# Kernel optimization log

Hardware: AMD Instinct MI355X
Metric: run time of the kernel (lower is better)

## Reference

```python
import jax, jax.numpy as jnp
import numpy as np

EPS = 1e-5

def _bn(x, p):
    # p: (4, C) rows = gamma, beta, running_mean, running_var ; x: (B, C, H, W)
    g, b, m, v = p[0], p[1], p[2], p[3]
    sh = (1, -1, 1, 1)
    return (x - m.reshape(sh)) * (g.reshape(sh) * jax.lax.rsqrt(v.reshape(sh) + EPS)) + b.reshape(sh)

def _cba1(x, w, p):
    # 1x1 conv (no bias) + BN + ReLU
    return jax.nn.relu(_bn(jnp.einsum('oc,bchw->bohw', w, x), p))

def setup_inputs() -> dict:
    B, C, H, W = 2, 512, 128, 256
    CK, K, CO = 256, 19, 512
    key = jax.random.key(0)
    ks = jax.random.split(key, 10)
    def w(k, shape, fan):
        return jax.random.normal(k, shape, jnp.float32) * (fan ** -0.5)
    def bn(c):
        return jnp.stack([jnp.ones((c,), jnp.float32), jnp.zeros((c,), jnp.float32),
                          jnp.zeros((c,), jnp.float32), jnp.ones((c,), jnp.float32)])
    return {
        'x': jax.random.normal(ks[0], (B, C, H, W), jnp.float32),
        'proxy_feats': jax.random.normal(ks[1], (B, C, K, 1), jnp.float32),
        'wq1': w(ks[2], (CK, C), C),  'bnq1': bn(CK),
        'wq2': w(ks[3], (CK, CK), CK), 'bnq2': bn(CK),
        'wk1': w(ks[4], (CK, C), C),  'bnk1': bn(CK),
        'wk2': w(ks[5], (CK, CK), CK), 'bnk2': bn(CK),
        'wv':  w(ks[6], (CK, C), C),  'bnv':  bn(CK),
        'wout': w(ks[7], (C, CK), CK), 'bnout': bn(C),
        'wbot': w(ks[8], (CO, 2 * C, 3, 3), 2 * C * 9), 'bnbot': bn(CO),
    }

def reference(x, proxy_feats, wq1, wq2, wk1, wk2, wv, wout, wbot,
              bnq1, bnq2, bnk1, bnk2, bnv, bnout, bnbot):
    B, C, H, W = x.shape
    CK = wq1.shape[0]
    # --- ObjectContextBlock: pixel-region cross attention ---
    q = _cba1(_cba1(x, wq1, bnq1), wq2, bnq2)            # (B, CK, H, W)
    k = _cba1(_cba1(proxy_feats, wk1, bnk1), wk2, bnk2)  # (B, CK, K, 1)
    v = _cba1(proxy_feats, wv, bnv)                      # (B, CK, K, 1)
    q = q.reshape(B, CK, H * W)                          # (B, CK, N)
    k = k.reshape(B, CK, -1)                             # (B, CK, K)
    v = v.reshape(B, CK, -1)                             # (B, CK, K)
    sim = jnp.einsum('bcn,bck->bnk', q, k) * (CK ** -0.5)
    sim = jax.nn.softmax(sim, axis=-1)                   # (B, N, K)
    ctx = jnp.einsum('bnk,bck->bcn', sim, v).reshape(B, CK, H, W)
    ctx = _cba1(ctx, wout, bnout)                        # (B, C, H, W)
    # --- bottleneck: concat + 3x3 conv + BN + ReLU ---
    cat = jnp.concatenate([ctx, x], axis=1)              # (B, 2C, H, W)
    out = jax.lax.conv_general_dilated(cat, wbot, (1, 1), 'SAME',
                                       dimension_numbers=('NCHW', 'OIHW', 'NCHW'))
    return jax.nn.relu(_bn(out, bnbot))
```

## Files before the change

kernel.cpp:

```cpp
#include <hip/hip_runtime.h>
#include <cstdint>

#define EPS 1e-5f
#define PADW 258
#define PADROWS 33540
#define NPIX 32768

typedef __attribute__((ext_vector_type(8))) short bf16x8;
typedef __attribute__((ext_vector_type(4))) float f32x4;

__device__ __forceinline__ ushort f2bf(float f) {
  union { float f; uint32_t u; } v; v.f = f;
  uint32_t r = v.u + 0x7fffu + ((v.u >> 16) & 1u);
  return (ushort)(r >> 16);
}
__device__ __forceinline__ float bf2f(ushort h) {
  union { uint32_t u; float f; } v; v.u = ((uint32_t)h) << 16;
  return v.f;
}
__device__ __forceinline__ void gload_lds16(const void* g, void* lds) {
  __builtin_amdgcn_global_load_lds((__attribute__((address_space(1))) void*)g,
                                   (__attribute__((address_space(3))) void*)lds,
                                   16, 0, 0);
}

template <int BMODE, int OMODE>
__global__ __launch_bounds__(256) void mfma_gemm(
    const ushort* __restrict__ A, const ushort* __restrict__ B,
    const float* __restrict__ bn, void* __restrict__ OutV,
    int M, int K, int pitchB, int ciB, long strideB, int pitchO, long strideO) {
  const int lane = threadIdx.x & 63;
  const int wave = threadIdx.x >> 6;
  const int wm = (wave & 1) * 64;
  const int wn = (wave >> 1) * 64;
  const int m0 = blockIdx.y * 128;
  const int n0 = blockIdx.x * 128;
  const int z  = blockIdx.z;
  B += (size_t)z * strideB;

  const int h = n0 >> 8, w0 = n0 & 255;
  long prowB;
  if (BMODE == 0) prowB = n0;
  else            prowB = (long)(h + 1) * PADW + (w0 + 1);

  __shared__ __align__(16) ushort Asl[4 * 128 * 8];
  __shared__ __align__(16) ushort Bsl[4 * 128 * 8];

  f32x4 acc[4][4];
#pragma unroll
  for (int mt = 0; mt < 4; ++mt)
#pragma unroll
    for (int nt = 0; nt < 4; ++nt) acc[mt][nt] = (f32x4){0.f, 0.f, 0.f, 0.f};

  for (int k0 = 0; k0 < K; k0 += 32) {
#pragma unroll
    for (int i = 0; i < 2; ++i) {
      int c = (wave * 2 + i) * 64 + lane;
      int mm = c >> 2, g = (c & 3) ^ ((mm >> 1) & 3);
      gload_lds16(A + (size_t)(m0 + mm) * K + (k0 + g * 8), Asl + c * 8);
    }
    long rowb; int cib;
    if (BMODE == 2) {
      int tap = k0 >> 10;
      int dy = tap / 3 - 1, dx = tap % 3 - 1;
      rowb = prowB + dy * PADW + dx;
      cib  = k0 & 1023;
    } else {
      rowb = prowB;
      cib  = ciB + k0;
    }
#pragma unroll
    for (int i = 0; i < 2; ++i) {
      int c = (wave * 2 + i) * 64 + lane;
      int nn = c >> 2, g = (c & 3) ^ ((nn >> 1) & 3);
      gload_lds16(B + (size_t)(rowb + nn) * pitchB + cib + g * 8, Bsl + c * 8);
    }
    __syncthreads();
    bf16x8 af[4], bfr[4];
#pragma unroll
    for (int t = 0; t < 4; ++t) {
      int ks = lane >> 4;
      int ma = wm + t * 16 + (lane & 15);
      int nb = wn + t * 16 + (lane & 15);
      af[t]  = *(const bf16x8*)(Asl + (ma * 4 + (ks ^ ((ma >> 1) & 3))) * 8);
      bfr[t] = *(const bf16x8*)(Bsl + (nb * 4 + (ks ^ ((nb >> 1) & 3))) * 8);
    }
#pragma unroll
    for (int mt = 0; mt < 4; ++mt)
#pragma unroll
      for (int nt = 0; nt < 4; ++nt)
        acc[mt][nt] = __builtin_amdgcn_mfma_f32_16x16x32_bf16(af[mt], bfr[nt], acc[mt][nt], 0, 0, 0);
    __syncthreads();
  }

  const int q4 = lane >> 4, col = lane & 15;
  float scv[16], bov[16];
#pragma unroll
  for (int mt = 0; mt < 4; ++mt)
#pragma unroll
    for (int r = 0; r < 4; ++r) {
      int m = m0 + wm + mt * 16 + q4 * 4 + r;
      float s = bn[m] * rsqrtf(bn[3 * M + m] + EPS);
      scv[mt * 4 + r] = s;
      bov[mt * 4 + r] = bn[M + m] - bn[2 * M + m] * s;
    }
  if (OMODE == 2) {
    float* Outf = (float*)OutV + (size_t)z * strideO;
#pragma unroll
    for (int mt = 0; mt < 4; ++mt)
#pragma unroll
      for (int r = 0; r < 4; ++r) {
        int m = m0 + wm + mt * 16 + q4 * 4 + r;
        float* rowp = Outf + (size_t)m * NPIX + n0 + wn;
#pragma unroll
        for (int nt = 0; nt < 4; ++nt)
          rowp[nt * 16 + col] = fmaxf(acc[mt][nt][r] * scv[mt * 4 + r] + bov[mt * 4 + r], 0.f);
      }
  } else {
    ushort* Outh = (ushort*)OutV + (size_t)z * strideO;
    long prowO = (OMODE == 0) ? (long)n0 : ((long)(h + 1) * PADW + (w0 + 1));
#pragma unroll
    for (int nt = 0; nt < 4; ++nt) {
      long row = prowO + wn + nt * 16 + col;
      ushort* p = Outh + (size_t)row * pitchO + m0 + wm;
#pragma unroll
      for (int mt = 0; mt < 4; ++mt) {
        ushort4 pk;
        pk.x = f2bf(fmaxf(acc[mt][nt][0] * scv[mt * 4 + 0] + bov[mt * 4 + 0], 0.f));
        pk.y = f2bf(fmaxf(acc[mt][nt][1] * scv[mt * 4 + 1] + bov[mt * 4 + 1], 0.f));
        pk.z = f2bf(fmaxf(acc[mt][nt][2] * scv[mt * 4 + 2] + bov[mt * 4 + 2], 0.f));
        pk.w = f2bf(fmaxf(acc[mt][nt][3] * scv[mt * 4 + 3] + bov[mt * 4 + 3], 0.f));
        *(ushort4*)(p + mt * 16 + q4 * 4) = pk;
      }
    }
  }
}

#define PXS  130
#define ROWC (PXS * 4)
#define BUFC (3 * ROWC)
__global__ __launch_bounds__(256, 3) void conv3x3_mfma(
    const ushort* __restrict__ W2, const ushort* __restrict__ cat,
    const float* __restrict__ bn, float* __restrict__ out) {
  const int tid  = threadIdx.x;
  const int lane = tid & 63;
  const int wave = tid >> 6;
  const int wm = (wave & 1) * 64;
  const int wn = (wave >> 1) * 64;
  const int m0 = (blockIdx.x & 3) * 128;
  const int n0 = (blockIdx.x >> 2) * 128;
  const int z  = blockIdx.z;
  const int h = n0 >> 8, w0 = n0 & 255;
  const int prow0 = (h + 1) * PADW + (w0 + 1);
  const ushort* Bz = cat + (size_t)z * PADROWS * 1024;

  __shared__ __align__(16) ushort halo[2 * BUFC * 8];

  f32x4 acc[4][4];
#pragma unroll
  for (int mt = 0; mt < 4; ++mt)
#pragma unroll
    for (int nt = 0; nt < 4; ++nt) acc[mt][nt] = (f32x4){0.f, 0.f, 0.f, 0.f};

  int offs[7];
#pragma unroll
  for (int s = 0; s < 7; ++s) {
    int c = s * 256 + tid;
    if (c < BUFC) {
      int o_slot = c & 3;
      int q = c >> 2;
      int p = q % PXS;
      int r = q / PXS;
      int o_g = o_slot ^ ((p >> 1) & 3);
      offs[s] = ((prow0 + (r - 1) * PADW + (p - 1)) << 10) + o_g * 8;
    } else {
      offs[s] = -1;
    }
  }

  auto stage = [&](int buf, int ci0n) {
#pragma unroll
    for (int s = 0; s < 7; ++s)
      if (offs[s] >= 0)
        gload_lds16(Bz + (size_t)offs[s] + ci0n,
                    halo + ((size_t)buf * BUFC + s * 256 + wave * 64) * 8);
  };

  const ushort* Alane = W2 + (size_t)(m0 + wm + (lane & 15)) * 32 + (lane >> 4) * 8;

  const int p0  = wn + (lane & 15);
  const int oct = lane >> 4;
  int hoff0[3];
#pragma unroll
  for (int dx = 0; dx < 3; ++dx) {
    int p = p0 + dx;
    hoff0[dx] = (p * 4 + (oct ^ ((p >> 1) & 3))) * 16;
  }

  stage(0, 0);
  __syncthreads();

  for (int it = 0; it < 32; ++it) {
    const ushort* Ait = Alane + (size_t)it * (9 * 16384);

    bf16x8 af[2][4];
#pragma unroll
    for (int t = 0; t < 2; ++t)
#pragma unroll
      for (int mt = 0; mt < 4; ++mt)
        af[t][mt] = *(const bf16x8*)(Ait + (size_t)t * 16384 + mt * 512);

    __builtin_amdgcn_sched_barrier(0);
    if (it < 31) stage((it + 1) & 1, (it + 1) * 32);
    __builtin_amdgcn_sched_barrier(0);

    const char* hb0 = (const char*)(halo + (size_t)(it & 1) * BUFC * 8);
    bf16x8 bfr[2][4];
#pragma unroll
    for (int nt = 0; nt < 4; ++nt)
      bfr[0][nt] = *(const bf16x8*)(hb0 + nt * 1024 + hoff0[0]);

#pragma unroll
    for (int t = 0; t < 9; ++t) {
      if (t < 8) {
        const int r1 = (t + 1) / 3, dx1 = (t + 1) % 3;
#pragma unroll
        for (int nt = 0; nt < 4; ++nt)
          bfr[(t + 1) & 1][nt] =
              *(const bf16x8*)(hb0 + r1 * (ROWC * 16) + nt * 1024 + hoff0[dx1]);
      }
      __builtin_amdgcn_s_setprio(1);
#pragma unroll
      for (int nt = 0; nt < 4; ++nt)
#pragma unroll
        for (int mt = 0; mt < 4; ++mt)
          acc[mt][nt] = __builtin_amdgcn_mfma_f32_16x16x32_bf16(
              af[t & 1][mt], bfr[t & 1][nt], acc[mt][nt], 0, 0, 0);
      __builtin_amdgcn_s_setprio(0);
      if (t < 7) {
#pragma unroll
        for (int mt = 0; mt < 4; ++mt)
          af[t & 1][mt] = *(const bf16x8*)(Ait + (size_t)(t + 2) * 16384 + mt * 512);
      }
    }
    __syncthreads();
  }

  const int q4 = lane >> 4, col = lane & 15;
  float* Outf = out + (size_t)z * 512 * NPIX;
#pragma unroll
  for (int mt = 0; mt < 4; ++mt)
#pragma unroll
    for (int r = 0; r < 4; ++r) {
      int m = m0 + wm + mt * 16 + q4 * 4 + r;
      float s  = bn[m] * rsqrtf(bn[3 * 512 + m] + EPS);
      float bo = bn[512 + m] - bn[2 * 512 + m] * s;
      float* rowp = Outf + (size_t)m * NPIX + n0 + wn;
#pragma unroll
      for (int nt = 0; nt < 4; ++nt)
        rowp[nt * 16 + col] = fmaxf(acc[mt][nt][r] * s + bo, 0.f);
    }
}

__global__ __launch_bounds__(64) void small_gemm_kernel(
    const float* __restrict__ Wm, const float* __restrict__ X,
    const float* __restrict__ bn, float* __restrict__ Y,
    int CO, int CI, int KC) {
  int co = blockIdx.x, b = blockIdx.y, kc = threadIdx.x;
  if (kc >= KC) return;
  const float* Xb = X + (size_t)b * CI * KC;
  float acc = 0.f;
  for (int c = 0; c < CI; ++c) acc += Wm[(size_t)co * CI + c] * Xb[(size_t)c * KC + kc];
  float s  = bn[co] * rsqrtf(bn[3 * CO + co] + EPS);
  float bs = bn[CO + co] - bn[2 * CO + co] * s;
  Y[((size_t)b * CO + co) * KC + kc] = fmaxf(acc * s + bs, 0.f);
}

__global__ __launch_bounds__(256) void attention_kernel(
    const ushort* __restrict__ qT, const float* __restrict__ Kp,
    const float* __restrict__ Vp, ushort* __restrict__ ctxT) {
  int b = blockIdx.y;
  int pix = blockIdx.x * 256 + threadIdx.x;
  __shared__ float ks[256][19], vs[256][19];
  for (int idx = threadIdx.x; idx < 256 * 19; idx += 256) {
    int c = idx / 19, kk = idx % 19;
    ks[c][kk] = Kp[((size_t)b * 256 + c) * 19 + kk];
    vs[c][kk] = Vp[((size_t)b * 256 + c) * 19 + kk];
  }
  __syncthreads();

  const ushort* qrow = qT + ((size_t)b * NPIX + pix) * 256;
  float sim[19];
#pragma unroll
  for (int kk = 0; kk < 19; ++kk) sim[kk] = 0.f;
  for (int c0 = 0; c0 < 256; c0 += 8) {
    uint4 raw = *(const uint4*)(qrow + c0);
    float qf[8] = {bf2f((ushort)(raw.x & 0xffff)), bf2f((ushort)(raw.x >> 16)),
                   bf2f((ushort)(raw.y & 0xffff)), bf2f((ushort)(raw.y >> 16)),
                   bf2f((ushort)(raw.z & 0xffff)), bf2f((ushort)(raw.z >> 16)),
                   bf2f((ushort)(raw.w & 0xffff)), bf2f((ushort)(raw.w >> 16))};
#pragma unroll
    for (int j = 0; j < 8; ++j)
#pragma unroll
      for (int kk = 0; kk < 19; ++kk) sim[kk] += qf[j] * ks[c0 + j][kk];
  }
  const float scale = 0.0625f;
  float mx = -1e30f;
#pragma unroll
  for (int kk = 0; kk < 19; ++kk) { sim[kk] *= scale; mx = fmaxf(mx, sim[kk]); }
  float denom = 0.f;
#pragma unroll
  for (int kk = 0; kk < 19; ++kk) { sim[kk] = __expf(sim[kk] - mx); denom += sim[kk]; }
  float inv = 1.f / denom;
#pragma unroll
  for (int kk = 0; kk < 19; ++kk) sim[kk] *= inv;

  ushort* crow = ctxT + ((size_t)b * NPIX + pix) * 256;
  for (int c0 = 0; c0 < 256; c0 += 8) {
    uint32_t o[4];
#pragma unroll
    for (int j = 0; j < 4; ++j) {
      float v0 = 0.f, v1 = 0.f;
#pragma unroll
      for (int kk = 0; kk < 19; ++kk) {
        v0 += sim[kk] * vs[c0 + j * 2][kk];
        v1 += sim[kk] * vs[c0 + j * 2 + 1][kk];
      }
      o[j] = (uint32_t)f2bf(v0) | ((uint32_t)f2bf(v1) << 16);
    }
    *(uint4*)(crow + c0) = make_uint4(o[0], o[1], o[2], o[3]);
  }
}

__global__ __launch_bounds__(256) void transpose_x_kernel(
    const float* __restrict__ x, ushort* __restrict__ cat) {
  int b = blockIdx.z, ci0 = blockIdx.y * 64, n0 = blockIdx.x * 64;
  __shared__ float t[64][65];
  const float* xb = x + ((size_t)b * 512 + ci0) * NPIX + n0;
  for (int i = 0; i < 16; ++i) {
    int idx = i * 256 + threadIdx.x;
    int c = idx >> 6, w = idx & 63;
    t[c][w] = xb[(size_t)c * NPIX + w];
  }
  __syncthreads();
  int h = n0 >> 8, w0 = n0 & 255;
  size_t pbase = ((size_t)b * PADROWS + (size_t)(h + 1) * PADW + (w0 + 1)) * 1024 + 512 + ci0;
  for (int i = 0; i < 16; ++i) {
    int idx = i * 256 + threadIdx.x;
    int n = idx >> 6, c = idx & 63;
    cat[pbase + (size_t)n * 1024 + c] = f2bf(t[c][n]);
  }
}

__global__ void convert_w_kernel(const float* __restrict__ in, ushort* __restrict__ out, int n) {
  int i = blockIdx.x * 256 + threadIdx.x;
  if (i < n) out[i] = f2bf(in[i]);
}
__global__ void repack_conv_w_kernel(const float* __restrict__ wbot, ushort* __restrict__ Wrb) {
  int idx = blockIdx.x * 256 + threadIdx.x;
  if (idx >= 512 * 9216) return;
  int ci_in = idx & 31;
  int r  = idx >> 5;
  int co = r & 511;
  int tt = r >> 9;
  int t = tt % 9, chunk = tt / 9;
  Wrb[idx] = f2bf(wbot[((size_t)co * 1024 + chunk * 32 + ci_in) * 9 + t]);
}

extern "C" void kernel_launch(void* const* d_in, const int* in_sizes, int n_in,
                              void* d_out, int out_size, void* d_ws, size_t ws_size,
                              hipStream_t stream) {
  const float* x     = (const float*)d_in[0];
  const float* proxy = (const float*)d_in[1];
  const float* wq1   = (const float*)d_in[2];
  const float* bnq1  = (const float*)d_in[3];
  const float* wq2   = (const float*)d_in[4];
  const float* bnq2  = (const float*)d_in[5];
  const float* wk1   = (const float*)d_in[6];
  const float* bnk1  = (const float*)d_in[7];
  const float* wk2   = (const float*)d_in[8];
  const float* bnk2  = (const float*)d_in[9];
  const float* wv    = (const float*)d_in[10];
  const float* bnv   = (const float*)d_in[11];
  const float* wout  = (const float*)d_in[12];
  const float* bnout = (const float*)d_in[13];
  const float* wbot  = (const float*)d_in[14];
  const float* bnbot = (const float*)d_in[15];
  float* out = (float*)d_out;

  const int B = 2, C = 512, CK = 256, KC = 19;
  char* ws = (char*)d_ws;
  const size_t catBytes = (size_t)B * PADROWS * 1024 * 2;
  ushort* cat  = (ushort*)ws;
  ushort* bufA = (ushort*)(ws + 137379840);
  ushort* bufB = (ushort*)(ws + 137379840 + 33554432);
  ushort* Wrb  = (ushort*)(ws + 204488704);
  ushort* wq1b = (ushort*)(ws + 213925888);
  ushort* wq2b = (ushort*)(ws + 214188032);
  ushort* woutb= (ushort*)(ws + 214319104);
  float*  k1   = (float*)(ws + 214581248);
  float*  k2   = k1 + (size_t)B * CK * KC;
  float*  vv   = k2 + (size_t)B * CK * KC;

  hipMemsetAsync(cat, 0, catBytes, stream);

  convert_w_kernel<<<(CK * C + 255) / 256, 256, 0, stream>>>(wq1, wq1b, CK * C);
  convert_w_kernel<<<(CK * CK + 255) / 256, 256, 0, stream>>>(wq2, wq2b, CK * CK);
  convert_w_kernel<<<(C * CK + 255) / 256, 256, 0, stream>>>(wout, woutb, C * CK);
  repack_conv_w_kernel<<<(512 * 9216 + 255) / 256, 256, 0, stream>>>(wbot, Wrb);

  small_gemm_kernel<<<dim3(CK, B), 64, 0, stream>>>(wk1, proxy, bnk1, k1, CK, C, KC);
  small_gemm_kernel<<<dim3(CK, B), 64, 0, stream>>>(wk2, k1, bnk2, k2, CK, CK, KC);
  small_gemm_kernel<<<dim3(CK, B), 64, 0, stream>>>(wv, proxy, bnv, vv, CK, C, KC);

  transpose_x_kernel<<<dim3(NPIX / 64, 8, B), 256, 0, stream>>>(x, cat);

  const long padStride = (long)PADROWS * 1024;
  const long nckStride = (long)NPIX * 256;

  mfma_gemm<1, 0><<<dim3(NPIX / 128, 2, B), 256, 0, stream>>>(
      wq1b, cat, bnq1, bufA, 256, 512, 1024, 512, padStride, 256, nckStride);
  mfma_gemm<0, 0><<<dim3(NPIX / 128, 2, B), 256, 0, stream>>>(
      wq2b, bufA, bnq2, bufB, 256, 256, 256, 0, nckStride, 256, nckStride);

  attention_kernel<<<dim3(NPIX / 256, B), 256, 0, stream>>>(bufB, k2, vv, bufA);

  mfma_gemm<0, 1><<<dim3(NPIX / 128, 4, B), 256, 0, stream>>>(
      woutb, bufA, bnout, cat, 512, 256, 256, 0, nckStride, 1024, padStride);

  conv3x3_mfma<<<dim3((NPIX / 128) * 4, 1, B), 256, 0, stream>>>(Wrb, cat, bnbot, out);
}
```

Measured before the change: 1.276 ms.

## Interleave conv halo staging per tap, zero only borders, split small GEMM reduction

The 3x3 conv main loop now spreads the seven async global-to-LDS halo loads across the first seven taps and uses fine-grained s_barrier plus explicit waitcnt in place of a bulk stage and a __syncthreads per chunk. It also prefetches the next chunk's weight fragments at the last tap. The full memset of the padded concat buffer is replaced by a small kernel that zeroes only the border pixels, since the interior is overwritten anyway. The small proxy GEMMs are split four ways over the input channels, with a reduction through shared memory. The extra per-tap barriers add synchronisation cost, and the hand-placed vmcnt values must match the number of outstanding loads to stay correct.

```diff
diff --git a/kernel.cpp b/kernel.cpp
--- a/kernel.cpp
+++ b/kernel.cpp
@@ -178,12 +178,10 @@
     }
   }
 
-  auto stage = [&](int buf, int ci0n) {
-#pragma unroll
-    for (int s = 0; s < 7; ++s)
-      if (offs[s] >= 0)
-        gload_lds16(Bz + (size_t)offs[s] + ci0n,
-                    halo + ((size_t)buf * BUFC + s * 256 + wave * 64) * 8);
+  auto stage1 = [&](int s, int buf, int ci0n) {
+    if (offs[s] >= 0)
+      gload_lds16(Bz + (size_t)offs[s] + ci0n,
+                  halo + ((size_t)buf * BUFC + s * 256 + wave * 64) * 8);
   };
 
   const ushort* Alane = W2 + (size_t)(m0 + wm + (lane & 15)) * 32 + (lane >> 4) * 8;
@@ -197,53 +195,63 @@
     hoff0[dx] = (p * 4 + (oct ^ ((p >> 1) & 3))) * 16;
   }
 
-  stage(0, 0);
-  __syncthreads();
+#pragma unroll
+  for (int s = 0; s < 7; ++s) stage1(s, 0, 0);
+  bf16x8 af[2][4];
+#pragma unroll
+  for (int t = 0; t < 2; ++t)
+#pragma unroll
+    for (int mt = 0; mt < 4; ++mt)
+      af[t][mt] = *(const bf16x8*)(Alane + (size_t)t * 16384 + mt * 512);
+  asm volatile("s_waitcnt vmcnt(8)" ::: "memory");
+  __builtin_amdgcn_sched_barrier(0);
+  __builtin_amdgcn_s_barrier();
 
   for (int it = 0; it < 32; ++it) {
     const ushort* Ait = Alane + (size_t)it * (9 * 16384);
-
-    bf16x8 af[2][4];
-#pragma unroll
-    for (int t = 0; t < 2; ++t)
-#pragma unroll
-      for (int mt = 0; mt < 4; ++mt)
-        af[t][mt] = *(const bf16x8*)(Ait + (size_t)t * 16384 + mt * 512);
-
-    __builtin_amdgcn_sched_barrier(0);
-    if (it < 31) stage((it + 1) & 1, (it + 1) * 32);
-    __builtin_amdgcn_sched_barrier(0);
-
+    const ushort* An  = Ait + (size_t)(9 * 16384);
     const char* hb0 = (const char*)(halo + (size_t)(it & 1) * BUFC * 8);
-    bf16x8 bfr[2][4];
-#pragma unroll
-    for (int nt = 0; nt < 4; ++nt)
-      bfr[0][nt] = *(const bf16x8*)(hb0 + nt * 1024 + hoff0[0]);
+    const int nbuf = (it + 1) & 1;
+    const int nci  = (it + 1) * 32;
+    const bool more = (it < 31);
 
 #pragma unroll
     for (int t = 0; t < 9; ++t) {
-      if (t < 8) {
-        const int r1 = (t + 1) / 3, dx1 = (t + 1) % 3;
-#pragma unroll
-        for (int nt = 0; nt < 4; ++nt)
-          bfr[(t + 1) & 1][nt] =
-              *(const bf16x8*)(hb0 + r1 * (ROWC * 16) + nt * 1024 + hoff0[dx1]);
-      }
+      const int r = t / 3, dx = t % 3;
+      bf16x8 bfr[4];
+#pragma unroll
+      for (int nt = 0; nt < 4; ++nt)
+        bfr[nt] = *(const bf16x8*)(hb0 + r * (ROWC * 16) + nt * 1024 + hoff0[dx]);
+      if (t < 7 && more) stage1(t, nbuf, nci);
+      __builtin_amdgcn_s_barrier();
+      asm volatile("s_waitcnt lgkmcnt(0)" ::: "memory");
+      __builtin_amdgcn_sched_barrier(0);
       __builtin_amdgcn_s_setprio(1);
 #pragma unroll
       for (int nt = 0; nt < 4; ++nt)
 #pragma unroll
         for (int mt = 0; mt < 4; ++mt)
           acc[mt][nt] = __builtin_amdgcn_mfma_f32_16x16x32_bf16(
-              af[t & 1][mt], bfr[t & 1][nt], acc[mt][nt], 0, 0, 0);
+              af[t & 1][mt], bfr[nt], acc[mt][nt], 0, 0, 0);
       __builtin_amdgcn_s_setprio(0);
       if (t < 7) {
 #pragma unroll
         for (int mt = 0; mt < 4; ++mt)
           af[t & 1][mt] = *(const bf16x8*)(Ait + (size_t)(t + 2) * 16384 + mt * 512);
+      } else if (t == 8 && more) {
+#pragma unroll
+        for (int mt = 0; mt < 4; ++mt)
+          af[0][mt] = *(const bf16x8*)(An + mt * 512);
+#pragma unroll
+        for (int mt = 0; mt < 4; ++mt)
+          af[1][mt] = *(const bf16x8*)(An + 16384 + mt * 512);
       }
-    }
-    __syncthreads();
+      if (t == 8) {
+        asm volatile("s_waitcnt vmcnt(8)" ::: "memory");
+        __builtin_amdgcn_sched_barrier(0);
+      }
+      __builtin_amdgcn_s_barrier();
+    }
   }
 
   const int q4 = lane >> 4, col = lane & 15;
@@ -262,18 +270,29 @@
     }
 }
 
-__global__ __launch_bounds__(64) void small_gemm_kernel(
+__global__ __launch_bounds__(256) void small_gemm_kernel(
     const float* __restrict__ Wm, const float* __restrict__ X,
     const float* __restrict__ bn, float* __restrict__ Y,
     int CO, int CI, int KC) {
-  int co = blockIdx.x, b = blockIdx.y, kc = threadIdx.x;
-  if (kc >= KC) return;
+  int co = blockIdx.x, b = blockIdx.y;
+  int q = threadIdx.x >> 6, kc = threadIdx.x & 63;
+  __shared__ float part[3][24];
   const float* Xb = X + (size_t)b * CI * KC;
+  const float* Wr = Wm + (size_t)co * CI;
   float acc = 0.f;
-  for (int c = 0; c < CI; ++c) acc += Wm[(size_t)co * CI + c] * Xb[(size_t)c * KC + kc];
-  float s  = bn[co] * rsqrtf(bn[3 * CO + co] + EPS);
-  float bs = bn[CO + co] - bn[2 * CO + co] * s;
-  Y[((size_t)b * CO + co) * KC + kc] = fmaxf(acc * s + bs, 0.f);
+  int cq = CI >> 2;
+  if (kc < KC) {
+    for (int c = q * cq; c < (q + 1) * cq; ++c)
+      acc += Wr[c] * Xb[(size_t)c * KC + kc];
+  }
+  if (q > 0 && kc < KC) part[q - 1][kc] = acc;
+  __syncthreads();
+  if (q == 0 && kc < KC) {
+    acc += part[0][kc] + part[1][kc] + part[2][kc];
+    float s  = bn[co] * rsqrtf(bn[3 * CO + co] + EPS);
+    float bs = bn[CO + co] - bn[2 * CO + co] * s;
+    Y[((size_t)b * CO + co) * KC + kc] = fmaxf(acc * s + bs, 0.f);
+  }
 }
 
 __global__ __launch_bounds__(256) void attention_kernel(
@@ -350,6 +369,18 @@
     int n = idx >> 6, c = idx & 63;
     cat[pbase + (size_t)n * 1024 + c] = f2bf(t[c][n]);
   }
+}
+
+__global__ __launch_bounds__(256) void zero_border_kernel(ushort* __restrict__ cat) {
+  int b = blockIdx.y, i = blockIdx.x;
+  int row, col;
+  if (i < 258)      { row = 0;            col = i; }
+  else if (i < 516) { row = 129;          col = i - 258; }
+  else if (i < 644) { row = i - 516 + 1;  col = 0; }
+  else              { row = i - 644 + 1;  col = 257; }
+  size_t base = ((size_t)b * PADROWS + (size_t)row * PADW + col) * 1024 +
+                (size_t)threadIdx.x * 4;
+  *(ushort4*)(cat + base) = make_ushort4(0, 0, 0, 0);
 }
 
 __global__ void convert_w_kernel(const float* __restrict__ in, ushort* __restrict__ out, int n) {
@@ -390,7 +421,6 @@
 
   const int B = 2, C = 512, CK = 256, KC = 19;
   char* ws = (char*)d_ws;
-  const size_t catBytes = (size_t)B * PADROWS * 1024 * 2;
   ushort* cat  = (ushort*)ws;
   ushort* bufA = (ushort*)(ws + 137379840);
   ushort* bufB = (ushort*)(ws + 137379840 + 33554432);
@@ -402,16 +432,16 @@
   float*  k2   = k1 + (size_t)B * CK * KC;
   float*  vv   = k2 + (size_t)B * CK * KC;
 
-  hipMemsetAsync(cat, 0, catBytes, stream);
+  zero_border_kernel<<<dim3(772, B), 256, 0, stream>>>(cat);
 
   convert_w_kernel<<<(CK * C + 255) / 256, 256, 0, stream>>>(wq1, wq1b, CK * C);
   convert_w_kernel<<<(CK * CK + 255) / 256, 256, 0, stream>>>(wq2, wq2b, CK * CK);
   convert_w_kernel<<<(C * CK + 255) / 256, 256, 0, stream>>>(wout, woutb, C * CK);
   repack_conv_w_kernel<<<(512 * 9216 + 255) / 256, 256, 0, stream>>>(wbot, Wrb);
 
-  small_gemm_kernel<<<dim3(CK, B), 64, 0, stream>>>(wk1, proxy, bnk1, k1, CK, C, KC);
-  small_gemm_kernel<<<dim3(CK, B), 64, 0, stream>>>(wk2, k1, bnk2, k2, CK, CK, KC);
-  small_gemm_kernel<<<dim3(CK, B), 64, 0, stream>>>(wv, proxy, bnv, vv, CK, C, KC);
+  small_gemm_kernel<<<dim3(CK, B), 256, 0, stream>>>(wk1, proxy, bnk1, k1, CK, C, KC);
+  small_gemm_kernel<<<dim3(CK, B), 256, 0, stream>>>(wk2, k1, bnk2, k2, CK, CK, KC);
+  small_gemm_kernel<<<dim3(CK, B), 256, 0, stream>>>(wv, proxy, bnv, vv, CK, C, KC);
 
   transpose_x_kernel<<<dim3(NPIX / 64, 8, B), 256, 0, stream>>>(x, cat);
 
```

Result: faster. 1.105 ms (-13.5%).
